# Kernel optimization log

Measured on AMD Instinct MI355X. Metric: run time of the kernel, lower is better.

## Reference

```python
import jax, jax.numpy as jnp
import numpy as np

H = W = 64      # input_resolution
WS = 8          # window_size
SS = 4          # shift_size
DIM = 96
HEADS = 4
HEAD_DIM = DIM // HEADS
SCALE = HEAD_DIM ** -0.5
N = WS * WS     # tokens per window
EPS = 1e-5


def _rel_pos_index():
    # static (N, N) int index into the (2*WS-1)^2 bias table
    coords = np.stack(np.meshgrid(np.arange(WS), np.arange(WS), indexing='ij'))  # (2, WS, WS)
    cf = coords.reshape(2, -1)                       # (2, N)
    rel = (cf[:, :, None] - cf[:, None, :]).transpose(1, 2, 0)  # (N, N, 2)
    rel[:, :, 0] += WS - 1
    rel[:, :, 1] += WS - 1
    rel[:, :, 0] *= 2 * WS - 1
    return rel.sum(-1)                               # (N, N)


def _attn_mask():
    # static (nW, N, N) 0/-100 mask for shifted windows
    img = np.zeros((H, W))
    cnt = 0
    sl = (slice(0, -WS), slice(-WS, -SS), slice(-SS, None))
    for hs in sl:
        for ws_ in sl:
            img[hs, ws_] = cnt
            cnt += 1
    mw = img.reshape(H // WS, WS, W // WS, WS).transpose(0, 2, 1, 3).reshape(-1, N)
    diff = mw[:, None, :] - mw[:, :, None]
    return np.where(diff != 0, -100.0, 0.0).astype(np.float32)


_RPI = jnp.asarray(_rel_pos_index())
_MASK = jnp.asarray(_attn_mask())  # (nW, N, N)


def _layernorm(x, g, b):
    mu = jnp.mean(x, axis=-1, keepdims=True)
    var = jnp.mean(jnp.square(x - mu), axis=-1, keepdims=True)
    return (x - mu) * jax.lax.rsqrt(var + EPS) * g + b


def setup_inputs() -> dict:
    key = jax.random.key(0)
    ks = jax.random.split(key, 8)
    s = 0.02
    return {
        'x': jax.random.normal(ks[0], (64, H * W, DIM), jnp.float32),
        'norm1_g': jnp.ones((DIM,), jnp.float32),
        'norm1_b': jnp.zeros((DIM,), jnp.float32),
        'qkv_w': jax.random.normal(ks[1], (3 * DIM, DIM), jnp.float32) * s,
        'qkv_b': jnp.zeros((3 * DIM,), jnp.float32),
        'rel_bias_table': jax.random.normal(ks[2], ((2 * WS - 1) ** 2, HEADS), jnp.float32) * s,
        'proj_w': jax.random.normal(ks[3], (DIM, DIM), jnp.float32) * s,
        'proj_b': jnp.zeros((DIM,), jnp.float32),
        'norm2_g': jnp.ones((DIM,), jnp.float32),
        'norm2_b': jnp.zeros((DIM,), jnp.float32),
        'fc1_w': jax.random.normal(ks[4], (4 * DIM, DIM), jnp.float32) * s,
        'fc1_b': jnp.zeros((4 * DIM,), jnp.float32),
        'fc2_w': jax.random.normal(ks[5], (DIM, 4 * DIM), jnp.float32) * s,
        'fc2_b': jnp.zeros((DIM,), jnp.float32),
    }


def reference(x, norm1_g, norm1_b, qkv_w, qkv_b, rel_bias_table, proj_w, proj_b,
              norm2_g, norm2_b, fc1_w, fc1_b, fc2_w, fc2_b):
    B, L, C = x.shape
    nW = (H // WS) * (W // WS)
    shortcut = x

    h = _layernorm(x, norm1_g, norm1_b).reshape(B, H, W, C)
    h = jnp.roll(h, (-SS, -SS), axis=(1, 2))
    # window partition -> (B*nW, N, C)
    h = h.reshape(B, H // WS, WS, W // WS, WS, C).transpose(0, 1, 3, 2, 4, 5)
    h = h.reshape(B * nW, N, C)

    qkv = h @ qkv_w.T + qkv_b                                   # (B_, N, 3C)
    qkv = qkv.reshape(B * nW, N, 3, HEADS, HEAD_DIM).transpose(2, 0, 3, 1, 4)
    q, k, v = qkv[0] * SCALE, qkv[1], qkv[2]                    # (B_, heads, N, hd)

    attn = jnp.einsum('whnd,whmd->whnm', q, k)                  # (B_, heads, N, N)
    bias = rel_bias_table[_RPI.reshape(-1)].reshape(N, N, HEADS).transpose(2, 0, 1)
    attn = attn + bias[None]
    attn = attn.reshape(B, nW, HEADS, N, N) + _MASK[None, :, None]
    attn = jax.nn.softmax(attn.reshape(B * nW, HEADS, N, N), axis=-1)

    out = jnp.einsum('whnm,whmd->whnd', attn, v)                # (B_, heads, N, hd)
    out = out.transpose(0, 2, 1, 3).reshape(B * nW, N, C)
    out = out @ proj_w.T + proj_b

    # window reverse + un-shift
    out = out.reshape(B, H // WS, W // WS, WS, WS, C).transpose(0, 1, 3, 2, 4, 5)
    out = out.reshape(B, H, W, C)
    out = jnp.roll(out, (SS, SS), axis=(1, 2)).reshape(B, L, C)

    x = shortcut + out
    h2 = _layernorm(x, norm2_g, norm2_b)
    h2 = jax.nn.gelu(h2 @ fc1_w.T + fc1_b, approximate=False)
    h2 = h2 @ fc2_w.T + fc2_b
    return x + h2
```

## Files before the change

### kernel.cpp

```cpp
#include <hip/hip_runtime.h>
#include <hip/hip_fp16.h>
#include <math.h>

typedef _Float16 half_t;
typedef _Float16 half8 __attribute__((ext_vector_type(8)));
typedef float f32x4 __attribute__((ext_vector_type(4)));

#define MFMA(a, b, c) __builtin_amdgcn_mfma_f32_16x16x32_f16((a), (b), (c), 0, 0, 0)

static constexpr float kScale = 0.2041241452319315f;
static constexpr int RS   = 104;
static constexpr int QSTR = 200;
static constexpr int VTS  = 72;
static constexpr int PS   = 72;
static constexpr int H1S  = 392;

__global__ __launch_bounds__(256) void k_convert(const float* __restrict__ qkv_w,
                                                 const float* __restrict__ proj_w,
                                                 const float* __restrict__ fc1_w,
                                                 const float* __restrict__ fc2_w,
                                                 half_t* __restrict__ wbuf) {
  int i = blockIdx.x * 256 + threadIdx.x;
  if (i < 27648)       wbuf[i] = (half_t)qkv_w[i];
  else if (i < 36864)  wbuf[i] = (half_t)proj_w[i - 27648];
  else if (i < 73728)  wbuf[i] = (half_t)fc1_w[i - 36864];
  else                 wbuf[i] = (half_t)fc2_w[i - 73728];
}

__global__ __launch_bounds__(256, 2) void k_swin(
    const float* __restrict__ x,
    const float* __restrict__ n1g, const float* __restrict__ n1b,
    const half_t* __restrict__ qkvw, const float* __restrict__ qkv_b,
    const float* __restrict__ tbl_g, const half_t* __restrict__ projw,
    const float* __restrict__ proj_b,
    const float* __restrict__ n2g, const float* __restrict__ n2b,
    const half_t* __restrict__ fc1w, const float* __restrict__ fc1b,
    const half_t* __restrict__ fc2w, const float* __restrict__ fc2b,
    float* __restrict__ out) {
  __shared__ __attribute__((aligned(16))) unsigned char smem[76800];
  half_t* resid = (half_t*)smem;
  unsigned char* U = smem + 13312;
  half_t* qbuf = (half_t*)U;
  half_t* vT   = (half_t*)(U + 25600);
  half_t* pbuf = (half_t*)(U + 39424);
  half_t* hn   = (half_t*)(U + 39424);
  float*  tblf = (float*)(U + 57856);
  int*    regb = (int*)(U + 61504);
  half_t* h1   = (half_t*)U;
  half_t* xn   = (half_t*)(U + 50176);

  int tid = threadIdx.x;
  int wave = tid >> 6, lane = tid & 63;
  int l15 = lane & 15, quad = lane >> 4;
  int blk = blockIdx.x;
  int bb = blk >> 6, wh = (blk >> 3) & 7, ww = blk & 7;

  for (int i = tid; i < 900; i += 256) tblf[(i & 3) * 228 + (i >> 2)] = tbl_g[i];
  if (tid < 64) {
    int ih = tid >> 3, iw = tid & 7;
    int rr = wh * 8 + ih, cc = ww * 8 + iw;
    regb[tid] = ((rr < 56) ? 0 : ((rr < 60) ? 1 : 2)) * 3 + ((cc < 56) ? 0 : ((cc < 60) ? 1 : 2));
  }

  {
    int tok = wave * 16 + l15;
    float gg[24], bv[24];
#pragma unroll
    for (int kt = 0; kt < 3; ++kt) {
      int c0 = kt * 32 + quad * 8;
      float4 g0 = *(const float4*)(n1g + c0);
      float4 g1 = *(const float4*)(n1g + c0 + 4);
      float4 b0 = *(const float4*)(n1b + c0);
      float4 b1 = *(const float4*)(n1b + c0 + 4);
      gg[kt*8+0]=g0.x; gg[kt*8+1]=g0.y; gg[kt*8+2]=g0.z; gg[kt*8+3]=g0.w;
      gg[kt*8+4]=g1.x; gg[kt*8+5]=g1.y; gg[kt*8+6]=g1.z; gg[kt*8+7]=g1.w;
      bv[kt*8+0]=b0.x; bv[kt*8+1]=b0.y; bv[kt*8+2]=b0.z; bv[kt*8+3]=b0.w;
      bv[kt*8+4]=b1.x; bv[kt*8+5]=b1.y; bv[kt*8+6]=b1.z; bv[kt*8+7]=b1.w;
    }
    int sr = (wh * 8 + (tok >> 3) + 4) & 63;
    int sc = (ww * 8 + (tok & 7) + 4) & 63;
    const float* rp = x + ((size_t)bb * 4096 + sr * 64 + sc) * 96;
    float v[24];
    float s1 = 0.f, s2 = 0.f;
#pragma unroll
    for (int kt = 0; kt < 3; ++kt) {
      float4 a = *(const float4*)(rp + kt * 32 + quad * 8);
      float4 b = *(const float4*)(rp + kt * 32 + quad * 8 + 4);
      v[kt*8+0]=a.x; v[kt*8+1]=a.y; v[kt*8+2]=a.z; v[kt*8+3]=a.w;
      v[kt*8+4]=b.x; v[kt*8+5]=b.y; v[kt*8+6]=b.z; v[kt*8+7]=b.w;
    }
#pragma unroll
    for (int c = 0; c < 24; ++c) { s1 += v[c]; s2 += v[c] * v[c]; }
    s1 += __shfl_xor(s1, 16); s1 += __shfl_xor(s1, 32);
    s2 += __shfl_xor(s2, 16); s2 += __shfl_xor(s2, 32);
    float mu = s1 * (1.f / 96.f);
    float inv = rsqrtf(fmaxf(s2 * (1.f / 96.f) - mu * mu, 0.f) + 1e-5f);
#pragma unroll
    for (int kt = 0; kt < 3; ++kt) {
      half8 hh, rr;
#pragma unroll
      for (int j = 0; j < 8; ++j) {
        float val = v[kt*8+j];
        rr[j] = (half_t)val;
        hh[j] = (half_t)((val - mu) * inv * gg[kt*8+j] + bv[kt*8+j]);
      }
      *(half8*)(&resid[tok * RS + kt * 32 + quad * 8]) = rr;
      *(half8*)(&hn[tok * RS + kt * 32 + quad * 8]) = hh;
    }
  }
  __syncthreads();

  {
    half8 af[4][3];
#pragma unroll
    for (int g = 0; g < 4; ++g)
#pragma unroll
      for (int kt = 0; kt < 3; ++kt)
        af[g][kt] = *(const half8*)(&hn[(g * 16 + l15) * RS + kt * 32 + quad * 8]);
    for (int t = wave; t < 18; t += 4) {
      half8 bf[3];
#pragma unroll
      for (int kt = 0; kt < 3; ++kt)
        bf[kt] = *(const half8*)(qkvw + (size_t)(t * 16 + l15) * 96 + kt * 32 + quad * 8);
      f32x4 acc[4] = {{0,0,0,0},{0,0,0,0},{0,0,0,0},{0,0,0,0}};
#pragma unroll
      for (int kt = 0; kt < 3; ++kt)
#pragma unroll
        for (int g = 0; g < 4; ++g)
          acc[g] = MFMA(af[g][kt], bf[kt], acc[g]);
      int col = t * 16 + l15;
      float bias = qkv_b[col];
      if (t < 12) {
        float sc_ = (t < 6) ? kScale : 1.f;
#pragma unroll
        for (int g = 0; g < 4; ++g)
#pragma unroll
          for (int r = 0; r < 4; ++r)
            qbuf[(g * 16 + quad * 4 + r) * QSTR + col] = (half_t)((acc[g][r] + bias) * sc_);
      } else {
        int vc = col - 192;
        int hd = vc / 24, c = vc - hd * 24;
#pragma unroll
        for (int g = 0; g < 4; ++g)
#pragma unroll
          for (int r = 0; r < 4; ++r)
            vT[hd * 24 * VTS + c * VTS + g * 16 + quad * 4 + r] = (half_t)(acc[g][r] + bias);
      }
    }
  }
  __syncthreads();

  f32x4 oacc[2][2][2];
  float inv_[4][4];
  {
    int head = wave;
    const half8 z8 = {};
    half8 qa[4], kb[4], vb[2][2];
#pragma unroll
    for (int g = 0; g < 4; ++g) {
      half8 t = *(const half8*)(&qbuf[(g * 16 + l15) * QSTR + head * 24 + quad * 8]);
      qa[g] = (quad < 3) ? t : z8;
    }
#pragma unroll
    for (int nt = 0; nt < 4; ++nt) {
      half8 t = *(const half8*)(&qbuf[(nt * 16 + l15) * QSTR + 96 + head * 24 + quad * 8]);
      kb[nt] = (quad < 3) ? t : z8;
    }
#pragma unroll
    for (int nt = 0; nt < 2; ++nt)
#pragma unroll
      for (int kt = 0; kt < 2; ++kt)
        vb[nt][kt] = *(const half8*)(&vT[head * 24 * VTS + (nt * 16 + l15) * VTS + kt * 32 + quad * 8]);

    float s[4][4][4];
#pragma unroll
    for (int g = 0; g < 4; ++g)
#pragma unroll
      for (int nt = 0; nt < 4; ++nt) {
        f32x4 a = {0, 0, 0, 0};
        a = MFMA(qa[g], kb[nt], a);
#pragma unroll
        for (int r = 0; r < 4; ++r) s[g][nt][r] = a[r];
      }

    int rj[4], jh_[4], jw_[4];
#pragma unroll
    for (int nt = 0; nt < 4; ++nt) {
      int j = nt * 16 + l15;
      rj[nt] = regb[j]; jh_[nt] = j >> 3; jw_[nt] = j & 7;
    }
#pragma unroll
    for (int g = 0; g < 4; ++g)
#pragma unroll
      for (int r = 0; r < 4; ++r) {
        int i = g * 16 + quad * 4 + r;
        int ih = i >> 3, iw = i & 7;
        int ri = regb[i];
#pragma unroll
        for (int nt = 0; nt < 4; ++nt) {
          float val = s[g][nt][r] + tblf[head * 228 + (ih - jh_[nt] + 7) * 15 + (iw - jw_[nt] + 7)];
          if (ri != rj[nt]) val -= 100.f;
          s[g][nt][r] = val;
        }
        float mx = fmaxf(fmaxf(s[g][0][r], s[g][1][r]), fmaxf(s[g][2][r], s[g][3][r]));
        mx = fmaxf(mx, __shfl_xor(mx, 1));
        mx = fmaxf(mx, __shfl_xor(mx, 2));
        mx = fmaxf(mx, __shfl_xor(mx, 4));
        mx = fmaxf(mx, __shfl_xor(mx, 8));
        float sum = 0.f;
#pragma unroll
        for (int nt = 0; nt < 4; ++nt) {
          float e = __expf(s[g][nt][r] - mx);
          s[g][nt][r] = e;
          sum += e;
        }
        sum += __shfl_xor(sum, 1);
        sum += __shfl_xor(sum, 2);
        sum += __shfl_xor(sum, 4);
        sum += __shfl_xor(sum, 8);
        inv_[g][r] = 1.f / sum;
      }

    half_t* pb = pbuf + head * 32 * PS;
#pragma unroll
    for (int hv = 0; hv < 2; ++hv) {
#pragma unroll
      for (int g2 = 0; g2 < 2; ++g2) {
        int g = hv * 2 + g2;
#pragma unroll
        for (int nt = 0; nt < 4; ++nt)
#pragma unroll
          for (int r = 0; r < 4; ++r)
            pb[(g2 * 16 + quad * 4 + r) * PS + nt * 16 + l15] = (half_t)s[g][nt][r];
      }
#pragma unroll
      for (int g2 = 0; g2 < 2; ++g2) {
        half8 pa[2];
#pragma unroll
        for (int kt = 0; kt < 2; ++kt)
          pa[kt] = *(const half8*)(&pb[(g2 * 16 + l15) * PS + kt * 32 + quad * 8]);
#pragma unroll
        for (int nt = 0; nt < 2; ++nt) {
          f32x4 a = {0, 0, 0, 0};
#pragma unroll
          for (int kt = 0; kt < 2; ++kt) a = MFMA(pa[kt], vb[nt][kt], a);
          oacc[hv][g2][nt] = a;
        }
      }
    }
  }
  __syncthreads();
  {
    int head = wave;
#pragma unroll
    for (int hv = 0; hv < 2; ++hv)
#pragma unroll
      for (int g2 = 0; g2 < 2; ++g2)
#pragma unroll
        for (int nt = 0; nt < 2; ++nt)
#pragma unroll
          for (int r = 0; r < 4; ++r) {
            int c = nt * 16 + l15;
            if (c < 24)
              qbuf[(hv * 32 + g2 * 16 + quad * 4 + r) * QSTR + head * 24 + c] =
                  (half_t)(oacc[hv][g2][nt][r] * inv_[hv * 2 + g2][r]);
          }
  }
  __syncthreads();

  {
    half8 pa2[4][3];
#pragma unroll
    for (int g = 0; g < 4; ++g)
#pragma unroll
      for (int kt = 0; kt < 3; ++kt)
        pa2[g][kt] = *(const half8*)(&qbuf[(g * 16 + l15) * QSTR + kt * 32 + quad * 8]);
    for (int t = wave; t < 6; t += 4) {
      half8 bf[3];
#pragma unroll
      for (int kt = 0; kt < 3; ++kt)
        bf[kt] = *(const half8*)(projw + (size_t)(t * 16 + l15) * 96 + kt * 32 + quad * 8);
      f32x4 acc[4] = {{0,0,0,0},{0,0,0,0},{0,0,0,0},{0,0,0,0}};
#pragma unroll
      for (int kt = 0; kt < 3; ++kt)
#pragma unroll
        for (int g = 0; g < 4; ++g)
          acc[g] = MFMA(pa2[g][kt], bf[kt], acc[g]);
      int col = t * 16 + l15;
      float bias = proj_b[col];
#pragma unroll
      for (int g = 0; g < 4; ++g)
#pragma unroll
        for (int r = 0; r < 4; ++r) {
          int row = g * 16 + quad * 4 + r;
          float rv = (float)resid[row * RS + col] + acc[g][r] + bias;
          resid[row * RS + col] = (half_t)rv;
        }
    }
  }
  __syncthreads();

  {
    int r4 = wave * 16 + (lane >> 2);
    int ch = lane & 3;
    const half_t* rp = resid + r4 * RS + ch * 24;
    half8 w0 = *(const half8*)(rp);
    half8 w1 = *(const half8*)(rp + 8);
    half8 w2 = *(const half8*)(rp + 16);
    float v[24];
#pragma unroll
    for (int j = 0; j < 8; ++j) {
      v[j] = (float)w0[j]; v[j + 8] = (float)w1[j]; v[j + 16] = (float)w2[j];
    }
    float s1 = 0.f, s2 = 0.f;
#pragma unroll
    for (int j = 0; j < 24; ++j) { s1 += v[j]; s2 += v[j] * v[j]; }
    s1 += __shfl_xor(s1, 1); s1 += __shfl_xor(s1, 2);
    s2 += __shfl_xor(s2, 1); s2 += __shfl_xor(s2, 2);
    float mu = s1 * (1.f / 96.f);
    float inv = rsqrtf(fmaxf(s2 * (1.f / 96.f) - mu * mu, 0.f) + 1e-5f);
    float gv[24], bb2[24];
#pragma unroll
    for (int q = 0; q < 6; ++q) {
      float4 g4 = *(const float4*)(n2g + ch * 24 + q * 4);
      float4 b4 = *(const float4*)(n2b + ch * 24 + q * 4);
      gv[q*4+0]=g4.x; gv[q*4+1]=g4.y; gv[q*4+2]=g4.z; gv[q*4+3]=g4.w;
      bb2[q*4+0]=b4.x; bb2[q*4+1]=b4.y; bb2[q*4+2]=b4.z; bb2[q*4+3]=b4.w;
    }
    half_t* op = xn + r4 * RS + ch * 24;
#pragma unroll
    for (int q = 0; q < 3; ++q) {
      half8 h;
#pragma unroll
      for (int j = 0; j < 8; ++j)
        h[j] = (half_t)((v[q*8+j] - mu) * inv * gv[q*8+j] + bb2[q*8+j]);
      *(half8*)(op + q * 8) = h;
    }
  }
  __syncthreads();

  {
    half8 a5[4][3];
#pragma unroll
    for (int g = 0; g < 4; ++g)
#pragma unroll
      for (int kt = 0; kt < 3; ++kt)
        a5[g][kt] = *(const half8*)(&xn[(g * 16 + l15) * RS + kt * 32 + quad * 8]);
    for (int t = wave; t < 24; t += 4) {
      int n0 = t * 16 + l15;
      half8 bf[3];
#pragma unroll
      for (int kt = 0; kt < 3; ++kt)
        bf[kt] = *(const half8*)(fc1w + (size_t)n0 * 96 + kt * 32 + quad * 8);
      f32x4 acc[4] = {{0,0,0,0},{0,0,0,0},{0,0,0,0},{0,0,0,0}};
#pragma unroll
      for (int kt = 0; kt < 3; ++kt)
#pragma unroll
        for (int g = 0; g < 4; ++g)
          acc[g] = MFMA(a5[g][kt], bf[kt], acc[g]);
      float bias = fc1b[n0];
#pragma unroll
      for (int g = 0; g < 4; ++g)
#pragma unroll
        for (int r = 0; r < 4; ++r) {
          float vv = acc[g][r] + bias;
          vv = 0.5f * vv * (1.f + erff(vv * 0.70710678118f));
          h1[(g * 16 + quad * 4 + r) * H1S + n0] = (half_t)vv;
        }
    }
  }
  __syncthreads();

  {
    int rt = wave;
    half8 a2[12];
#pragma unroll
    for (int kt = 0; kt < 12; ++kt)
      a2[kt] = *(const half8*)(&h1[(rt * 16 + l15) * H1S + kt * 32 + quad * 8]);
#pragma unroll
    for (int t = 0; t < 6; ++t) {
      f32x4 acc = {0, 0, 0, 0};
#pragma unroll
      for (int kt = 0; kt < 12; ++kt) {
        half8 bf = *(const half8*)(fc2w + (size_t)(t * 16 + l15) * 384 + kt * 32 + quad * 8);
        acc = MFMA(a2[kt], bf, acc);
      }
      int col = t * 16 + l15;
      float bias = fc2b[col];
#pragma unroll
      for (int r = 0; r < 4; ++r) {
        int tok = rt * 16 + quad * 4 + r;
        int sr = (wh * 8 + (tok >> 3) + 4) & 63;
        int sc = (ww * 8 + (tok & 7) + 4) & 63;
        size_t fidx = ((size_t)bb * 4096 + sr * 64 + sc) * 96 + col;
        out[fidx] = (float)resid[tok * RS + col] + acc[r] + bias;
      }
    }
  }
}

extern "C" void kernel_launch(void* const* d_in, const int* in_sizes, int n_in,
                              void* d_out, int out_size, void* d_ws, size_t ws_size,
                              hipStream_t stream) {
  const float* x      = (const float*)d_in[0];
  const float* n1g    = (const float*)d_in[1];
  const float* n1b    = (const float*)d_in[2];
  const float* qkv_w  = (const float*)d_in[3];
  const float* qkv_b  = (const float*)d_in[4];
  const float* rtbl   = (const float*)d_in[5];
  const float* proj_w = (const float*)d_in[6];
  const float* proj_b = (const float*)d_in[7];
  const float* n2g    = (const float*)d_in[8];
  const float* n2b    = (const float*)d_in[9];
  const float* fc1_w  = (const float*)d_in[10];
  const float* fc1_b  = (const float*)d_in[11];
  const float* fc2_w  = (const float*)d_in[12];
  const float* fc2_b  = (const float*)d_in[13];
  float* out = (float*)d_out;

  if (ws_size < 221184) return;
  half_t* wbuf = (half_t*)d_ws;

  k_convert<<<432, 256, 0, stream>>>(qkv_w, proj_w, fc1_w, fc2_w, wbuf);
  k_swin<<<4096, 256, 0, stream>>>(x, n1g, n1b, wbuf, qkv_b, rtbl,
                                   wbuf + 27648, proj_b, n2g, n2b,
                                   wbuf + 36864, fc1_b, wbuf + 73728, fc2_b, out);
}
```

Measured before the change: 473.9 us.

## Shrink LDS footprint to fit three blocks per CU

Shared memory per block drops from 76.8KB to about 52.7KB, and launch bounds rise to 3 blocks per CU. To get there, the fp16 residual buffer is removed and the shortcut is re-read from global x at the projection epilogue. The bias table and region IDs are now read or computed directly instead of staged in LDS. The P·V staging buffer is cut to 16 rows per head, and the MLP is split into two 32-token halves with extra barriers. This trades extra global reads, redundant index arithmetic and more synchronisation for higher occupancy; the tighter register budget may cause spills.

```diff
diff --git a/kernel.cpp b/kernel.cpp
--- a/kernel.cpp
+++ b/kernel.cpp
@@ -27,7 +27,7 @@
   else                 wbuf[i] = (half_t)fc2_w[i - 73728];
 }
 
-__global__ __launch_bounds__(256, 2) void k_swin(
+__global__ __launch_bounds__(256, 3) void k_swin(
     const float* __restrict__ x,
     const float* __restrict__ n1g, const float* __restrict__ n1b,
     const half_t* __restrict__ qkvw, const float* __restrict__ qkv_b,
@@ -37,30 +37,20 @@
     const half_t* __restrict__ fc1w, const float* __restrict__ fc1b,
     const half_t* __restrict__ fc2w, const float* __restrict__ fc2b,
     float* __restrict__ out) {
-  __shared__ __attribute__((aligned(16))) unsigned char smem[76800];
-  half_t* resid = (half_t*)smem;
-  unsigned char* U = smem + 13312;
-  half_t* qbuf = (half_t*)U;
-  half_t* vT   = (half_t*)(U + 25600);
-  half_t* pbuf = (half_t*)(U + 39424);
-  half_t* hn   = (half_t*)(U + 39424);
-  float*  tblf = (float*)(U + 57856);
-  int*    regb = (int*)(U + 61504);
-  half_t* h1   = (half_t*)U;
-  half_t* xn   = (half_t*)(U + 50176);
+  __shared__ __attribute__((aligned(16))) unsigned char smem[52736];
+  half_t* qbuf = (half_t*)smem;
+  half_t* h1h  = (half_t*)smem;
+  half_t* vT   = (half_t*)(smem + 25600);
+  half_t* rbuf = (half_t*)(smem + 25600);
+  half_t* hn   = (half_t*)(smem + 39424);
+  half_t* pbuf = (half_t*)(smem + 39424);
+  half_t* xn   = (half_t*)(smem + 39424);
 
   int tid = threadIdx.x;
   int wave = tid >> 6, lane = tid & 63;
   int l15 = lane & 15, quad = lane >> 4;
   int blk = blockIdx.x;
   int bb = blk >> 6, wh = (blk >> 3) & 7, ww = blk & 7;
-
-  for (int i = tid; i < 900; i += 256) tblf[(i & 3) * 228 + (i >> 2)] = tbl_g[i];
-  if (tid < 64) {
-    int ih = tid >> 3, iw = tid & 7;
-    int rr = wh * 8 + ih, cc = ww * 8 + iw;
-    regb[tid] = ((rr < 56) ? 0 : ((rr < 60) ? 1 : 2)) * 3 + ((cc < 56) ? 0 : ((cc < 60) ? 1 : 2));
-  }
 
   {
     int tok = wave * 16 + l15;
@@ -97,14 +87,10 @@
     float inv = rsqrtf(fmaxf(s2 * (1.f / 96.f) - mu * mu, 0.f) + 1e-5f);
 #pragma unroll
     for (int kt = 0; kt < 3; ++kt) {
-      half8 hh, rr;
-#pragma unroll
-      for (int j = 0; j < 8; ++j) {
-        float val = v[kt*8+j];
-        rr[j] = (half_t)val;
-        hh[j] = (half_t)((val - mu) * inv * gg[kt*8+j] + bv[kt*8+j]);
-      }
-      *(half8*)(&resid[tok * RS + kt * 32 + quad * 8]) = rr;
+      half8 hh;
+#pragma unroll
+      for (int j = 0; j < 8; ++j)
+        hh[j] = (half_t)((v[kt*8+j] - mu) * inv * gg[kt*8+j] + bv[kt*8+j]);
       *(half8*)(&hn[tok * RS + kt * 32 + quad * 8]) = hh;
     }
   }
@@ -150,7 +136,7 @@
   }
   __syncthreads();
 
-  f32x4 oacc[2][2][2];
+  f32x4 oacc[4][2];
   float inv_[4][4];
   {
     int head = wave;
@@ -187,7 +173,9 @@
 #pragma unroll
     for (int nt = 0; nt < 4; ++nt) {
       int j = nt * 16 + l15;
-      rj[nt] = regb[j]; jh_[nt] = j >> 3; jw_[nt] = j & 7;
+      jh_[nt] = j >> 3; jw_[nt] = j & 7;
+      int rr = wh * 8 + jh_[nt], cc = ww * 8 + jw_[nt];
+      rj[nt] = ((rr < 56) ? 0 : ((rr < 60) ? 1 : 2)) * 3 + ((cc < 56) ? 0 : ((cc < 60) ? 1 : 2));
     }
 #pragma unroll
     for (int g = 0; g < 4; ++g)
@@ -195,10 +183,12 @@
       for (int r = 0; r < 4; ++r) {
         int i = g * 16 + quad * 4 + r;
         int ih = i >> 3, iw = i & 7;
-        int ri = regb[i];
+        int rr = wh * 8 + ih, cc = ww * 8 + iw;
+        int ri = ((rr < 56) ? 0 : ((rr < 60) ? 1 : 2)) * 3 + ((cc < 56) ? 0 : ((cc < 60) ? 1 : 2));
 #pragma unroll
         for (int nt = 0; nt < 4; ++nt) {
-          float val = s[g][nt][r] + tblf[head * 228 + (ih - jh_[nt] + 7) * 15 + (iw - jw_[nt] + 7)];
+          float val = s[g][nt][r] +
+              tbl_g[((ih - jh_[nt] + 7) * 15 + (iw - jw_[nt] + 7)) * 4 + head];
           if (ri != rj[nt]) val -= 100.f;
           s[g][nt][r] = val;
         }
@@ -221,31 +211,24 @@
         inv_[g][r] = 1.f / sum;
       }
 
-    half_t* pb = pbuf + head * 32 * PS;
-#pragma unroll
-    for (int hv = 0; hv < 2; ++hv) {
-#pragma unroll
-      for (int g2 = 0; g2 < 2; ++g2) {
-        int g = hv * 2 + g2;
-#pragma unroll
-        for (int nt = 0; nt < 4; ++nt)
-#pragma unroll
-          for (int r = 0; r < 4; ++r)
-            pb[(g2 * 16 + quad * 4 + r) * PS + nt * 16 + l15] = (half_t)s[g][nt][r];
-      }
-#pragma unroll
-      for (int g2 = 0; g2 < 2; ++g2) {
-        half8 pa[2];
-#pragma unroll
-        for (int kt = 0; kt < 2; ++kt)
-          pa[kt] = *(const half8*)(&pb[(g2 * 16 + l15) * PS + kt * 32 + quad * 8]);
-#pragma unroll
-        for (int nt = 0; nt < 2; ++nt) {
-          f32x4 a = {0, 0, 0, 0};
-#pragma unroll
-          for (int kt = 0; kt < 2; ++kt) a = MFMA(pa[kt], vb[nt][kt], a);
-          oacc[hv][g2][nt] = a;
-        }
+    half_t* pb = pbuf + head * 16 * PS;
+#pragma unroll
+    for (int q4 = 0; q4 < 4; ++q4) {
+#pragma unroll
+      for (int nt = 0; nt < 4; ++nt)
+#pragma unroll
+        for (int r = 0; r < 4; ++r)
+          pb[(quad * 4 + r) * PS + nt * 16 + l15] = (half_t)s[q4][nt][r];
+      half8 pa[2];
+#pragma unroll
+      for (int kt = 0; kt < 2; ++kt)
+        pa[kt] = *(const half8*)(&pb[l15 * PS + kt * 32 + quad * 8]);
+#pragma unroll
+      for (int nt = 0; nt < 2; ++nt) {
+        f32x4 a = {0, 0, 0, 0};
+#pragma unroll
+        for (int kt = 0; kt < 2; ++kt) a = MFMA(pa[kt], vb[nt][kt], a);
+        oacc[q4][nt] = a;
       }
     }
   }
@@ -253,18 +236,16 @@
   {
     int head = wave;
 #pragma unroll
-    for (int hv = 0; hv < 2; ++hv)
-#pragma unroll
-      for (int g2 = 0; g2 < 2; ++g2)
-#pragma unroll
-        for (int nt = 0; nt < 2; ++nt)
-#pragma unroll
-          for (int r = 0; r < 4; ++r) {
-            int c = nt * 16 + l15;
-            if (c < 24)
-              qbuf[(hv * 32 + g2 * 16 + quad * 4 + r) * QSTR + head * 24 + c] =
-                  (half_t)(oacc[hv][g2][nt][r] * inv_[hv * 2 + g2][r]);
-          }
+    for (int q4 = 0; q4 < 4; ++q4)
+#pragma unroll
+      for (int nt = 0; nt < 2; ++nt)
+#pragma unroll
+        for (int r = 0; r < 4; ++r) {
+          int c = nt * 16 + l15;
+          if (c < 24)
+            qbuf[(q4 * 16 + quad * 4 + r) * QSTR + head * 24 + c] =
+                (half_t)(oacc[q4][nt][r] * inv_[q4][r]);
+        }
   }
   __syncthreads();
 
@@ -292,9 +273,11 @@
       for (int g = 0; g < 4; ++g)
 #pragma unroll
         for (int r = 0; r < 4; ++r) {
-          int row = g * 16 + quad * 4 + r;
-          float rv = (float)resid[row * RS + col] + acc[g][r] + bias;
-          resid[row * RS + col] = (half_t)rv;
+          int tok = g * 16 + quad * 4 + r;
+          int sr = (wh * 8 + (tok >> 3) + 4) & 63;
+          int sc = (ww * 8 + (tok & 7) + 4) & 63;
+          size_t fidx = ((size_t)bb * 4096 + sr * 64 + sc) * 96 + col;
+          rbuf[tok * RS + col] = (half_t)(x[fidx] + acc[g][r] + bias);
         }
     }
   }
@@ -303,7 +286,7 @@
   {
     int r4 = wave * 16 + (lane >> 2);
     int ch = lane & 3;
-    const half_t* rp = resid + r4 * RS + ch * 24;
+    const half_t* rp = rbuf + r4 * RS + ch * 24;
     half8 w0 = *(const half8*)(rp);
     half8 w1 = *(const half8*)(rp + 8);
     half8 w2 = *(const half8*)(rp + 16);
@@ -339,63 +322,66 @@
   }
   __syncthreads();
 
-  {
-    half8 a5[4][3];
-#pragma unroll
-    for (int g = 0; g < 4; ++g)
-#pragma unroll
-      for (int kt = 0; kt < 3; ++kt)
-        a5[g][kt] = *(const half8*)(&xn[(g * 16 + l15) * RS + kt * 32 + quad * 8]);
-    for (int t = wave; t < 24; t += 4) {
-      int n0 = t * 16 + l15;
-      half8 bf[3];
-#pragma unroll
-      for (int kt = 0; kt < 3; ++kt)
-        bf[kt] = *(const half8*)(fc1w + (size_t)n0 * 96 + kt * 32 + quad * 8);
-      f32x4 acc[4] = {{0,0,0,0},{0,0,0,0},{0,0,0,0},{0,0,0,0}};
-#pragma unroll
-      for (int kt = 0; kt < 3; ++kt)
-#pragma unroll
-        for (int g = 0; g < 4; ++g)
-          acc[g] = MFMA(a5[g][kt], bf[kt], acc[g]);
-      float bias = fc1b[n0];
-#pragma unroll
-      for (int g = 0; g < 4; ++g)
+  for (int hb = 0; hb < 2; ++hb) {
+    {
+      half8 a5[2][3];
+#pragma unroll
+      for (int g2 = 0; g2 < 2; ++g2)
+#pragma unroll
+        for (int kt = 0; kt < 3; ++kt)
+          a5[g2][kt] = *(const half8*)(&xn[((hb * 2 + g2) * 16 + l15) * RS + kt * 32 + quad * 8]);
+      for (int t = wave; t < 24; t += 4) {
+        int n0 = t * 16 + l15;
+        half8 bf[3];
+#pragma unroll
+        for (int kt = 0; kt < 3; ++kt)
+          bf[kt] = *(const half8*)(fc1w + (size_t)n0 * 96 + kt * 32 + quad * 8);
+        f32x4 acc[2] = {{0,0,0,0},{0,0,0,0}};
+#pragma unroll
+        for (int kt = 0; kt < 3; ++kt)
+#pragma unroll
+          for (int g2 = 0; g2 < 2; ++g2)
+            acc[g2] = MFMA(a5[g2][kt], bf[kt], acc[g2]);
+        float bias = fc1b[n0];
+#pragma unroll
+        for (int g2 = 0; g2 < 2; ++g2)
+#pragma unroll
+          for (int r = 0; r < 4; ++r) {
+            float vv = acc[g2][r] + bias;
+            vv = 0.5f * vv * (1.f + erff(vv * 0.70710678118f));
+            h1h[(g2 * 16 + quad * 4 + r) * H1S + n0] = (half_t)vv;
+          }
+      }
+    }
+    __syncthreads();
+    {
+      int rt = wave >> 1, chh = wave & 1;
+      half8 a2[12];
+#pragma unroll
+      for (int kt = 0; kt < 12; ++kt)
+        a2[kt] = *(const half8*)(&h1h[(rt * 16 + l15) * H1S + kt * 32 + quad * 8]);
+#pragma unroll
+      for (int i = 0; i < 3; ++i) {
+        int t = chh * 3 + i;
+        f32x4 acc = {0, 0, 0, 0};
+#pragma unroll
+        for (int kt = 0; kt < 12; ++kt) {
+          half8 bf = *(const half8*)(fc2w + (size_t)(t * 16 + l15) * 384 + kt * 32 + quad * 8);
+          acc = MFMA(a2[kt], bf, acc);
+        }
+        int col = t * 16 + l15;
+        float bias = fc2b[col];
 #pragma unroll
         for (int r = 0; r < 4; ++r) {
-          float vv = acc[g][r] + bias;
-          vv = 0.5f * vv * (1.f + erff(vv * 0.70710678118f));
-          h1[(g * 16 + quad * 4 + r) * H1S + n0] = (half_t)vv;
-        }
-    }
-  }
-  __syncthreads();
-
-  {
-    int rt = wave;
-    half8 a2[12];
-#pragma unroll
-    for (int kt = 0; kt < 12; ++kt)
-      a2[kt] = *(const half8*)(&h1[(rt * 16 + l15) * H1S + kt * 32 + quad * 8]);
-#pragma unroll
-    for (int t = 0; t < 6; ++t) {
-      f32x4 acc = {0, 0, 0, 0};
-#pragma unroll
-      for (int kt = 0; kt < 12; ++kt) {
-        half8 bf = *(const half8*)(fc2w + (size_t)(t * 16 + l15) * 384 + kt * 32 + quad * 8);
-        acc = MFMA(a2[kt], bf, acc);
-      }
-      int col = t * 16 + l15;
-      float bias = fc2b[col];
-#pragma unroll
-      for (int r = 0; r < 4; ++r) {
-        int tok = rt * 16 + quad * 4 + r;
-        int sr = (wh * 8 + (tok >> 3) + 4) & 63;
-        int sc = (ww * 8 + (tok & 7) + 4) & 63;
-        size_t fidx = ((size_t)bb * 4096 + sr * 64 + sc) * 96 + col;
-        out[fidx] = (float)resid[tok * RS + col] + acc[r] + bias;
-      }
-    }
+          int tok = hb * 32 + rt * 16 + quad * 4 + r;
+          int sr = (wh * 8 + (tok >> 3) + 4) & 63;
+          int sc = (ww * 8 + (tok & 7) + 4) & 63;
+          size_t fidx = ((size_t)bb * 4096 + sr * 64 + sc) * 96 + col;
+          out[fidx] = (float)rbuf[tok * RS + col] + acc[r] + bias;
+        }
+      }
+    }
+    __syncthreads();
   }
 }
 
```

New measurement: 438.8 us. -7.4%, faster.
